# Kernel tuning notes

Hardware: AMD Instinct MI355X
Metric: run time of the kernel (lower is better)

## Reference

```python
import jax, jax.numpy as jnp
import numpy as np
import math

NUM_BUCKETS = 32
MAX_DISTANCE = 128


def _relative_position_bucket(relative_position):
    # Unidirectional (bidirectional=False): rp = max(-relative_position, 0)
    rp = jnp.maximum(-relative_position, 0)
    max_exact = NUM_BUCKETS // 2  # 16
    is_small = rp < max_exact
    rp_f = jnp.maximum(rp, 1).astype(jnp.float32)
    large = max_exact + (
        jnp.log(rp_f / max_exact) / math.log(MAX_DISTANCE / max_exact)
        * (NUM_BUCKETS - max_exact)
    ).astype(jnp.int32)
    large = jnp.minimum(large, NUM_BUCKETS - 1)
    return jnp.where(is_small, rp, large)


def _t5_rel_bias(bias_table, T):
    # bias_table: [num_buckets, n_heads] -> [1, n_heads, T, T]
    ctx = jnp.arange(T, dtype=jnp.int32)[:, None]
    mem = jnp.arange(T, dtype=jnp.int32)[None, :]
    buckets = _relative_position_bucket(mem - ctx)  # [T, T]
    values = bias_table[buckets]  # [T, T, H]
    return jnp.transpose(values, (2, 0, 1))[None]  # [1, H, T, T]


def setup_inputs() -> dict:
    key = jax.random.key(0)
    ks = jax.random.split(key, 6)
    B, T, C, H = 2, 2048, 1024, 16
    x = jax.random.normal(ks[0], (B, T, C), dtype=jnp.float32)
    W_attn = jax.random.normal(ks[1], (C, 3 * C), dtype=jnp.float32) * 0.02
    b_attn = jnp.zeros((3 * C,), dtype=jnp.float32)
    W_proj = jax.random.normal(ks[2], (C, C), dtype=jnp.float32) * 0.02
    b_proj = jnp.zeros((C,), dtype=jnp.float32)
    bias_table = jax.random.normal(ks[3], (NUM_BUCKETS, H), dtype=jnp.float32) * 0.02
    return {"x": x, "W_attn": W_attn, "b_attn": b_attn,
            "W_proj": W_proj, "b_proj": b_proj, "bias_table": bias_table}


def reference(x, W_attn, b_attn, W_proj, b_proj, bias_table):
    B, T, C = x.shape
    H = bias_table.shape[1]
    D = C // H
    qkv = x @ W_attn + b_attn  # [B, T, 3C]
    q, k, v = jnp.split(qkv, 3, axis=-1)
    # [B, T, C] -> [B, H, T, D]
    q = q.reshape(B, T, H, D).transpose(0, 2, 1, 3)
    k = k.reshape(B, T, H, D).transpose(0, 2, 1, 3)
    v = v.reshape(B, T, H, D).transpose(0, 2, 1, 3)
    rel_bias = _t5_rel_bias(bias_table, T)  # [1, H, T, T]
    att = jnp.einsum('bhtd,bhsd->bhts', q, k) * (1.0 / math.sqrt(D))
    att = att + rel_bias
    causal = jnp.tril(jnp.ones((T, T), dtype=bool))
    att = jnp.where(causal, att, -jnp.inf)
    att = jax.nn.softmax(att, axis=-1)
    y = jnp.einsum('bhts,bhsd->bhtd', att, v)  # [B, H, T, D]
    y = y.transpose(0, 2, 1, 3).reshape(B, T, C)
    return y @ W_proj + b_proj
```

## Files before the change

kernel.cpp:

```cpp
#include <hip/hip_runtime.h>
#include <hip/hip_bf16.h>
#include <math.h>

typedef __attribute__((ext_vector_type(4))) float f32x4;
typedef __attribute__((ext_vector_type(16))) float f32x16;
typedef __attribute__((ext_vector_type(8))) __bf16 bf16x8;
typedef __attribute__((ext_vector_type(4))) __bf16 bf16x4;
typedef __attribute__((ext_vector_type(4))) unsigned int u32x4;
typedef __attribute__((ext_vector_type(2))) unsigned int u32x2;

#define DEVI __device__ __forceinline__

DEVI f32x4 mfma16(bf16x8 a, bf16x8 b, f32x4 c) {
  return __builtin_amdgcn_mfma_f32_16x16x32_bf16(a, b, c, 0, 0, 0);
}
DEVI f32x16 mfma32(bf16x8 a, bf16x8 b, f32x16 c) {
  return __builtin_amdgcn_mfma_f32_32x32x16_bf16(a, b, c, 0, 0, 0);
}

DEVI void gload16(const void* g, void* l) {
  __builtin_amdgcn_global_load_lds(
      (const __attribute__((address_space(1))) void*)g,
      (__attribute__((address_space(3))) void*)l, 16, 0, 0);
}

DEVI float exp2a(float x) {
  float r;
  asm("v_exp_f32 %0, %1" : "=v"(r) : "v"(x));
  return r;
}
DEVI unsigned cvtpk(float lo, float hi) {
  unsigned r;
  asm("v_cvt_pk_bf16_f32 %0, %1, %2" : "=v"(r) : "v"(lo), "v"(hi));
  return r;
}

#define LOG2E 1.4426950408889634f
#define QSCALE 0.18033688011110793f
#define FIXMAX 8.0f

__global__ __launch_bounds__(256) void prep_k(
    const float* __restrict__ x, const float* __restrict__ W_attn,
    const float* __restrict__ W_proj, const float* __restrict__ bt,
    __bf16* __restrict__ xb, __bf16* __restrict__ WaT,
    __bf16* __restrict__ WpT, float* __restrict__ tbl) {
  __shared__ float tile[32][33];
  int bid = blockIdx.x;
  const int t = threadIdx.x;
  if (bid < 4096) {
    int i = (bid * 256 + t) * 4;
    float4 v = *(const float4*)&x[i];
    bf16x4 o = {(__bf16)v.x, (__bf16)v.y, (__bf16)v.z, (__bf16)v.w};
    *(bf16x4*)&xb[i] = o;
    return;
  }
  bid -= 4096;
  if (bid < 4096) {
    const float* in;
    __bf16* out;
    int Cc, bx, by;
    if (bid < 3072) {
      in = W_attn; out = WaT; Cc = 3072; bx = bid % 96; by = bid / 96;
    } else {
      int b2 = bid - 3072;
      in = W_proj; out = WpT; Cc = 1024; bx = b2 % 32; by = b2 / 32;
    }
    const int R = 1024;
    int tx = t & 31, ty = t >> 5;
    int xcol = bx * 32 + tx;
    for (int r = ty; r < 32; r += 8)
      tile[r][tx] = in[(size_t)(by * 32 + r) * Cc + xcol];
    __syncthreads();
    int xo = by * 32 + tx;
    for (int r = ty; r < 32; r += 8)
      out[(size_t)(bx * 32 + r) * R + xo] = (__bf16)tile[tx][r];
    return;
  }
  bid -= 4096;
  int idx = bid * 256 + t;
  int h = idx >> 11, rp = idx & 2047;
  int bucket;
  if (rp < 16) {
    bucket = rp;
  } else {
    float v = (logf((float)rp * 0.0625f) / 2.0794415416798357f) * 16.0f;
    bucket = 16 + (int)v;
    if (bucket > 31) bucket = 31;
  }
  tbl[idx] = bt[bucket * 16 + h] * LOG2E;
}

__global__ __launch_bounds__(256) void gemm_qkv(
    const __bf16* __restrict__ A, const __bf16* __restrict__ BT,
    const float* __restrict__ bias,
    __bf16* __restrict__ qb, __bf16* __restrict__ kb, __bf16* __restrict__ vtb,
    int M, int N, int K) {
  __shared__ __align__(16) __bf16 lA[2][128 * 32];
  __shared__ __align__(16) __bf16 lB[2][128 * 32];
  const int t = threadIdx.x;
  const int w = t >> 6, lane = t & 63;
  const int m0 = blockIdx.x * 128, n0 = blockIdx.y * 128;
  const int wr = (w >> 1) * 64, wc = (w & 1) * 64;

  f32x4 acc[4][4] = {};

  const int rA = lane & 15;
  const int kk = (lane >> 4) * 8;

  auto STAGE = [&](int buf, int k0) {
#pragma unroll
    for (int r = 0; r < 2; ++r) {
      int c = r * 256 + t;
      int row = c >> 2, cc = c & 3;
      gload16(A + (size_t)(m0 + row) * K + k0 + cc * 8,
              &lA[buf][(r * 256 + w * 64) * 8]);
      gload16(BT + (size_t)(n0 + row) * K + k0 + cc * 8,
              &lB[buf][(r * 256 + w * 64) * 8]);
    }
  };

  STAGE(0, 0);
  int cur = 0;
  for (int k0 = 0; k0 < K; k0 += 32, cur ^= 1) {
    __syncthreads();
    if (k0 + 32 < K) STAGE(cur ^ 1, k0 + 32);
    bf16x8 af[4], bfr[4];
#pragma unroll
    for (int i = 0; i < 4; ++i)
      af[i] = *(const bf16x8*)&lA[cur][(wr + i * 16 + rA) * 32 + kk];
#pragma unroll
    for (int j = 0; j < 4; ++j)
      bfr[j] = *(const bf16x8*)&lB[cur][(wc + j * 16 + rA) * 32 + kk];
#pragma unroll
    for (int i = 0; i < 4; ++i)
#pragma unroll
      for (int j = 0; j < 4; ++j)
        acc[i][j] = mfma16(af[i], bfr[j], acc[i][j]);
  }

  const int colb = n0 + wc + rA;
  const int rowb = m0 + wr + (lane >> 4) * 4;
#pragma unroll
  for (int j = 0; j < 4; ++j) {
    int n = colb + j * 16;
    float bv = bias[n];
#pragma unroll
    for (int i = 0; i < 4; ++i) {
#pragma unroll
      for (int e = 0; e < 4; ++e) {
        int m = rowb + i * 16 + e;
        float v = acc[i][j][e] + bv;
        int b = m >> 11, tt = m & 2047;
        int sec = n >> 10, nn = n & 1023;
        int h = nn >> 6, d = nn & 63;
        if (sec == 0)
          qb[(((size_t)(b * 16 + h)) * 2048 + tt) * 64 + d] = (__bf16)(v * QSCALE);
        else if (sec == 1)
          kb[(((size_t)(b * 16 + h)) * 2048 + tt) * 64 + d] = (__bf16)v;
        else
          vtb[(((size_t)(b * 16 + h)) * 64 + d) * 2048 + tt] = (__bf16)v;
      }
    }
  }
}

__global__ __launch_bounds__(256) void gemm_proj(
    const __bf16* __restrict__ A, const __bf16* __restrict__ BT,
    const float* __restrict__ bias, float* __restrict__ outF,
    int M, int N, int K) {
  __shared__ __align__(16) __bf16 lA[2][64 * 32];
  __shared__ __align__(16) __bf16 lB[2][128 * 32];
  const int t = threadIdx.x;
  const int w = t >> 6, lane = t & 63;
  const int m0 = blockIdx.x * 64, n0 = blockIdx.y * 128;
  const int wr = (w >> 1) * 32, wc = (w & 1) * 64;

  f32x4 acc[2][4] = {};

  const int rA = lane & 15;
  const int kk = (lane >> 4) * 8;

  auto STAGE = [&](int buf, int k0) {
    {
      int row = t >> 2, cc = t & 3;
      gload16(A + (size_t)(m0 + row) * K + k0 + cc * 8,
              &lA[buf][(w * 64) * 8]);
    }
#pragma unroll
    for (int r = 0; r < 2; ++r) {
      int c = r * 256 + t;
      int row = c >> 2, cc = c & 3;
      gload16(BT + (size_t)(n0 + row) * K + k0 + cc * 8,
              &lB[buf][(r * 256 + w * 64) * 8]);
    }
  };

  STAGE(0, 0);
  int cur = 0;
  for (int k0 = 0; k0 < K; k0 += 32, cur ^= 1) {
    __syncthreads();
    if (k0 + 32 < K) STAGE(cur ^ 1, k0 + 32);
    bf16x8 af[2], bfr[4];
#pragma unroll
    for (int i = 0; i < 2; ++i)
      af[i] = *(const bf16x8*)&lA[cur][(wr + i * 16 + rA) * 32 + kk];
#pragma unroll
    for (int j = 0; j < 4; ++j)
      bfr[j] = *(const bf16x8*)&lB[cur][(wc + j * 16 + rA) * 32 + kk];
#pragma unroll
    for (int i = 0; i < 2; ++i)
#pragma unroll
      for (int j = 0; j < 4; ++j)
        acc[i][j] = mfma16(af[i], bfr[j], acc[i][j]);
  }

  const int colb = n0 + wc + rA;
  const int rowb = m0 + wr + (lane >> 4) * 4;
#pragma unroll
  for (int j = 0; j < 4; ++j) {
    int n = colb + j * 16;
    float bv = bias[n];
#pragma unroll
    for (int i = 0; i < 2; ++i) {
#pragma unroll
      for (int e = 0; e < 4; ++e) {
        int m = rowb + i * 16 + e;
        outF[(size_t)m * N + n] = acc[i][j][e] + bv;
      }
    }
  }
}

__global__ __launch_bounds__(256) void attn_k(
    const __bf16* __restrict__ q, const __bf16* __restrict__ k,
    const __bf16* __restrict__ vt, const float* __restrict__ tbl,
    __bf16* __restrict__ y) {
  __shared__ __align__(16) char smem[2 * 8192 + 2 * 8192 + 2 * 768];
  float* lbuf = (float*)(smem + 32768);

  const int t = threadIdx.x, w = t >> 6, lane = t & 63;
  const int bh = blockIdx.x, b = bh >> 4, h = bh & 15;
  const int qt64 = 31 - blockIdx.y;
  const int qs = w >> 1, ks = w & 1;
  const int ncol = lane & 31, hi = lane >> 5;
  const int swl = ncol & 7;

  const __bf16* qp = q + (size_t)bh * 2048 * 64;
  const __bf16* kp = k + (size_t)bh * 2048 * 64;
  const __bf16* vp = vt + (size_t)bh * 64 * 2048;
  const float* tb = tbl + h * 2048;
  const float bconst = tb[2047] - FIXMAX;

  bf16x8 qf[4];
  {
    const __bf16* qr = qp + (size_t)(qt64 * 64 + qs * 32 + ncol) * 64 + hi * 8;
#pragma unroll
    for (int dc = 0; dc < 4; ++dc) qf[dc] = *(const bf16x8*)(qr + dc * 16);
  }

  f32x16 O0 = {}, O1 = {};
  float lsum = 0.f;
  const int ibase = 95 + 32 * (qs - ks) - 4 * hi + ncol;

  auto STAGE = [&](int buf, int jt) {
#pragma unroll
    for (int r = 0; r < 2; ++r) {
      int c = r * 256 + t;
      int row = c >> 3, cc = c & 7;
      int sc = cc ^ (row & 7);
      gload16(kp + (size_t)(jt * 64 + row) * 64 + sc * 8,
              smem + buf * 8192 + (r * 256 + w * 64) * 16);
      gload16(vp + (size_t)row * 2048 + jt * 64 + sc * 8,
              smem + 16384 + buf * 8192 + (r * 256 + w * 64) * 16);
    }
    int dtj = qt64 - jt;
    if (dtj < 3 && t < 192) {
      int rb = dtj * 64 - 95 + t;
      lbuf[buf * 192 + t] = tb[rb < 0 ? 0 : rb] - FIXMAX;
    }
  };

  STAGE(0, 0);
  int cur = 0;
  for (int jt = 0; jt <= qt64; ++jt, cur ^= 1) {
    const int dt = qt64 - jt;
    const int rel = 2 * dt + qs - ks;
    __syncthreads();
    if (jt < qt64) STAGE(cur ^ 1, jt + 1);
    if (rel < 0) continue;

    const char* Kc = smem + cur * 8192;
    const char* Vc = smem + 16384 + cur * 8192;
    const float* lbc = lbuf + cur * 192;

    f32x16 s;
    if (rel >= 5) {
#pragma unroll
      for (int r = 0; r < 16; ++r) s[r] = bconst;
    } else {
#pragma unroll
      for (int r = 0; r < 16; ++r) {
        int cr8 = (r & 3) + 8 * (r >> 2);
        float v = lbc[ibase - cr8];
        if (rel == 0 && ncol < cr8 + 4 * hi) v = -1e30f;
        s[r] = v;
      }
    }
    const char* Kb = Kc + (ks * 32 + ncol) * 128;
#pragma unroll
    for (int dc = 0; dc < 4; ++dc) {
      bf16x8 kf = *(const bf16x8*)(Kb + (((dc * 2 + hi) ^ swl) << 4));
      s = mfma32(kf, qf[dc], s);
    }
    float p[16];
#pragma unroll
    for (int r = 0; r < 16; ++r) {
      p[r] = exp2a(s[r]);
      lsum += p[r];
    }
#pragma unroll
    for (int s16 = 0; s16 < 2; ++s16) {
      unsigned we0 = cvtpk(p[8 * s16 + 0], p[8 * s16 + 1]);
      unsigned we1 = cvtpk(p[8 * s16 + 2], p[8 * s16 + 3]);
      unsigned wo0 = cvtpk(p[8 * s16 + 4], p[8 * s16 + 5]);
      unsigned wo1 = cvtpk(p[8 * s16 + 6], p[8 * s16 + 7]);
      u32x2 r0 = __builtin_amdgcn_permlane32_swap(we0, wo0, false, false);
      u32x2 r1 = __builtin_amdgcn_permlane32_swap(we1, wo1, false, false);
      u32x4 aw = {r0[0], r1[0], r0[1], r1[1]};
      bf16x8 af = __builtin_bit_cast(bf16x8, aw);
#pragma unroll
      for (int db = 0; db < 2; ++db) {
        const char* Vb = Vc + (db * 32 + ncol) * 128;
        bf16x8 vf = *(const bf16x8*)(Vb +
            ((((ks * 2 + s16) * 2 + hi) ^ swl) << 4));
        if (db == 0) O0 = mfma32(af, vf, O0);
        else         O1 = mfma32(af, vf, O1);
      }
    }
  }

  lsum += __shfl_xor(lsum, 32);
  __syncthreads();
  float* ls = (float*)(smem + 32768);
  if (ks) {
    char* dst = smem + qs * 8192 + lane * 128;
#pragma unroll
    for (int c = 0; c < 4; ++c) {
      f32x4 v0 = {O0[4 * c], O0[4 * c + 1], O0[4 * c + 2], O0[4 * c + 3]};
      *(f32x4*)(dst + ((c ^ swl) << 4)) = v0;
      f32x4 v1 = {O1[4 * c], O1[4 * c + 1], O1[4 * c + 2], O1[4 * c + 3]};
      *(f32x4*)(dst + (((c + 4) ^ swl) << 4)) = v1;
    }
    ls[qs * 64 + lane] = lsum;
  }
  __syncthreads();
  if (!ks) {
    lsum += ls[qs * 64 + lane];
    const char* src = smem + qs * 8192 + lane * 128;
#pragma unroll
    for (int c = 0; c < 4; ++c) {
      f32x4 v0 = *(const f32x4*)(src + ((c ^ swl) << 4));
      f32x4 v1 = *(const f32x4*)(src + (((c + 4) ^ swl) << 4));
#pragma unroll
      for (int e = 0; e < 4; ++e) {
        O0[4 * c + e] += v0[e];
        O1[4 * c + e] += v1[e];
      }
    }
    float rinv = 1.0f / lsum;
#pragma unroll
    for (int r = 0; r < 16; ++r) {
      int cr = (r & 3) + 8 * (r >> 2) + 4 * hi;
      float ri = __shfl(rinv, cr);
      int row = qt64 * 64 + qs * 32 + cr;
      size_t base = ((size_t)(b * 2048 + row)) * 1024 + h * 64 + ncol;
      y[base]      = (__bf16)(O0[r] * ri);
      y[base + 32] = (__bf16)(O1[r] * ri);
    }
  }
}


extern "C" void kernel_launch(void* const* d_in, const int* in_sizes, int n_in,
                              void* d_out, int out_size, void* d_ws, size_t ws_size,
                              hipStream_t stream) {
  const float* x = (const float*)d_in[0];
  const float* W_attn = (const float*)d_in[1];
  const float* b_attn = (const float*)d_in[2];
  const float* W_proj = (const float*)d_in[3];
  const float* b_proj = (const float*)d_in[4];
  const float* bias_table = (const float*)d_in[5];
  float* out = (float*)d_out;

  char* ws = (char*)d_ws;
  __bf16* xb   = (__bf16*)(ws + 0);
  __bf16* WaT  = (__bf16*)(ws + 8388608);
  __bf16* WpT  = (__bf16*)(ws + 14680064);
  __bf16* qb   = (__bf16*)(ws + 16777216);
  __bf16* kb   = (__bf16*)(ws + 25165824);
  __bf16* vtb  = (__bf16*)(ws + 33554432);
  __bf16* yb   = (__bf16*)(ws + 41943040);
  float*  tbl  = (float*)(ws + 50331648);

  prep_k<<<8320, 256, 0, stream>>>(x, W_attn, W_proj, bias_table,
                                   xb, WaT, WpT, tbl);
  gemm_qkv<<<dim3(32, 24), 256, 0, stream>>>(xb, WaT, b_attn,
                                             qb, kb, vtb, 4096, 3072, 1024);
  attn_k<<<dim3(32, 32), 256, 0, stream>>>(qb, kb, vtb, tbl, yb);
  gemm_proj<<<dim3(64, 8), 256, 0, stream>>>(yb, WpT, b_proj, out,
                                             4096, 1024, 1024);
}
```

Baseline: 109.8 us.

## Rewrite QKV GEMM with 256x256 tiles, swizzled LDS and interleaved MFMA phases

Replaces the 128x128 QKV GEMM tile with a 256x256 block of 8 waves, a K step of 64 and 64KB per operand of double-buffered LDS using an XOR swizzle. The main loop is split into four barrier-separated phases that reload A/B fragments between MFMA bursts, raising wave priority during MFMA. The goal is more operand reuse per LDS byte and fewer bank conflicts. The cost is only 192 blocks for 256 CUs, so parallelism drops, and the tile size and problem shape are now hardcoded.

```diff
diff --git a/kernel.cpp b/kernel.cpp
--- a/kernel.cpp
+++ b/kernel.cpp
@@ -90,69 +90,143 @@
   tbl[idx] = bt[bucket * 16 + h] * LOG2E;
 }
 
-__global__ __launch_bounds__(256) void gemm_qkv(
+__global__ __launch_bounds__(512, 2) void gemm_qkv(
     const __bf16* __restrict__ A, const __bf16* __restrict__ BT,
     const float* __restrict__ bias,
-    __bf16* __restrict__ qb, __bf16* __restrict__ kb, __bf16* __restrict__ vtb,
-    int M, int N, int K) {
-  __shared__ __align__(16) __bf16 lA[2][128 * 32];
-  __shared__ __align__(16) __bf16 lB[2][128 * 32];
-  const int t = threadIdx.x;
-  const int w = t >> 6, lane = t & 63;
-  const int m0 = blockIdx.x * 128, n0 = blockIdx.y * 128;
-  const int wr = (w >> 1) * 64, wc = (w & 1) * 64;
-
-  f32x4 acc[4][4] = {};
-
+    __bf16* __restrict__ qb, __bf16* __restrict__ kb, __bf16* __restrict__ vtb) {
+  __shared__ __align__(16) char lAm[65536];
+  __shared__ __align__(16) char lBm[65536];
+  const int t = threadIdx.x, w = t >> 6, lane = t & 63;
+  const int wm = w >> 2, wn = w & 3;
+  const int m0 = blockIdx.x * 256, n0 = blockIdx.y * 256;
   const int rA = lane & 15;
-  const int kk = (lane >> 4) * 8;
-
-  auto STAGE = [&](int buf, int k0) {
-#pragma unroll
-    for (int r = 0; r < 2; ++r) {
-      int c = r * 256 + t;
-      int row = c >> 2, cc = c & 3;
-      gload16(A + (size_t)(m0 + row) * K + k0 + cc * 8,
-              &lA[buf][(r * 256 + w * 64) * 8]);
-      gload16(BT + (size_t)(n0 + row) * K + k0 + cc * 8,
-              &lB[buf][(r * 256 + w * 64) * 8]);
-    }
+  const int aoff = rA * 128 + (((lane >> 4) * 16) ^ ((rA & 4) ? 32 : 0));
+  const int bro = (wn & 1) * 8192;
+
+  int srw[2], scl[2];
+#pragma unroll
+  for (int r = 0; r < 2; ++r) {
+    int d = r * 8192 + w * 1024 + lane * 16;
+    int lg = d ^ ((lane & 32) ? 32 : 0);
+    srw[r] = lg >> 7;
+    scl[r] = (lg & 127) >> 1;
+  }
+
+  f32x4 acc[8][4] = {};
+
+  auto STG = [&](int buf, const __bf16* src, int rows0, int kk0, char* opm,
+                 int half) {
+#pragma unroll
+    for (int r = 0; r < 2; ++r)
+      gload16(src + (size_t)(rows0 + half * 128 + srw[r]) * 1024 + kk0 + scl[r],
+              opm + buf * 32768 + half * 16384 + r * 8192 + w * 1024);
   };
-
-  STAGE(0, 0);
-  int cur = 0;
-  for (int k0 = 0; k0 < K; k0 += 32, cur ^= 1) {
-    __syncthreads();
-    if (k0 + 32 < K) STAGE(cur ^ 1, k0 + 32);
-    bf16x8 af[4], bfr[4];
+  auto STGALL = [&](int buf, int kk0) {
+    STG(buf, A, m0, kk0, lAm, 0);
+    STG(buf, A, m0, kk0, lAm, 1);
+    STG(buf, BT, n0, kk0, lBm, 0);
+    STG(buf, BT, n0, kk0, lBm, 1);
+  };
+
+  STGALL(0, 0);
+  asm volatile("s_waitcnt vmcnt(0)" ::: "memory");
+  __builtin_amdgcn_s_barrier();
+
+  for (int kt = 0; kt < 16; ++kt) {
+    const int c = kt & 1;
+    const char* Ah = lAm + c * 32768 + wm * 16384;
+    const char* Bh = lBm + c * 32768 + (wn >> 1) * 16384 + bro;
+    bf16x8 af[4][2], bfr[2][2];
+
+#pragma unroll
+    for (int i = 0; i < 4; ++i) {
+      af[i][0] = *(const bf16x8*)(Ah + i * 2048 + aoff);
+      af[i][1] = *(const bf16x8*)(Ah + i * 2048 + 64 + aoff);
+    }
+#pragma unroll
+    for (int j = 0; j < 2; ++j) {
+      bfr[j][0] = *(const bf16x8*)(Bh + j * 2048 + aoff);
+      bfr[j][1] = *(const bf16x8*)(Bh + j * 2048 + 64 + aoff);
+    }
+    if (kt + 1 < 16) STGALL(c ^ 1, (kt + 1) * 64);
+    __builtin_amdgcn_s_barrier();
+    __builtin_amdgcn_s_setprio(1);
 #pragma unroll
     for (int i = 0; i < 4; ++i)
-      af[i] = *(const bf16x8*)&lA[cur][(wr + i * 16 + rA) * 32 + kk];
-#pragma unroll
-    for (int j = 0; j < 4; ++j)
-      bfr[j] = *(const bf16x8*)&lB[cur][(wc + j * 16 + rA) * 32 + kk];
+#pragma unroll
+      for (int j = 0; j < 2; ++j)
+#pragma unroll
+        for (int kc = 0; kc < 2; ++kc)
+          acc[i][j] = mfma16(af[i][kc], bfr[j][kc], acc[i][j]);
+    __builtin_amdgcn_s_setprio(0);
+    __builtin_amdgcn_s_barrier();
+
+#pragma unroll
+    for (int j = 0; j < 2; ++j) {
+      bfr[j][0] = *(const bf16x8*)(Bh + (2 + j) * 2048 + aoff);
+      bfr[j][1] = *(const bf16x8*)(Bh + (2 + j) * 2048 + 64 + aoff);
+    }
+    __builtin_amdgcn_s_barrier();
+    __builtin_amdgcn_s_setprio(1);
 #pragma unroll
     for (int i = 0; i < 4; ++i)
 #pragma unroll
-      for (int j = 0; j < 4; ++j)
-        acc[i][j] = mfma16(af[i], bfr[j], acc[i][j]);
-  }
-
-  const int colb = n0 + wc + rA;
-  const int rowb = m0 + wr + (lane >> 4) * 4;
+      for (int j = 0; j < 2; ++j)
+#pragma unroll
+        for (int kc = 0; kc < 2; ++kc)
+          acc[i][2 + j] = mfma16(af[i][kc], bfr[j][kc], acc[i][2 + j]);
+    __builtin_amdgcn_s_setprio(0);
+    __builtin_amdgcn_s_barrier();
+
+#pragma unroll
+    for (int i = 0; i < 4; ++i) {
+      af[i][0] = *(const bf16x8*)(Ah + (4 + i) * 2048 + aoff);
+      af[i][1] = *(const bf16x8*)(Ah + (4 + i) * 2048 + 64 + aoff);
+    }
+    __builtin_amdgcn_s_barrier();
+    __builtin_amdgcn_s_setprio(1);
+#pragma unroll
+    for (int i = 0; i < 4; ++i)
+#pragma unroll
+      for (int j = 0; j < 2; ++j)
+#pragma unroll
+        for (int kc = 0; kc < 2; ++kc)
+          acc[4 + i][2 + j] = mfma16(af[i][kc], bfr[j][kc], acc[4 + i][2 + j]);
+    __builtin_amdgcn_s_setprio(0);
+    __builtin_amdgcn_s_barrier();
+
+#pragma unroll
+    for (int j = 0; j < 2; ++j) {
+      bfr[j][0] = *(const bf16x8*)(Bh + j * 2048 + aoff);
+      bfr[j][1] = *(const bf16x8*)(Bh + j * 2048 + 64 + aoff);
+    }
+    __builtin_amdgcn_s_barrier();
+    __builtin_amdgcn_s_setprio(1);
+#pragma unroll
+    for (int i = 0; i < 4; ++i)
+#pragma unroll
+      for (int j = 0; j < 2; ++j)
+#pragma unroll
+        for (int kc = 0; kc < 2; ++kc)
+          acc[4 + i][j] = mfma16(af[i][kc], bfr[j][kc], acc[4 + i][j]);
+    __builtin_amdgcn_s_setprio(0);
+    if (kt + 1 < 16) asm volatile("s_waitcnt vmcnt(0)" ::: "memory");
+    __builtin_amdgcn_s_barrier();
+  }
+
 #pragma unroll
   for (int j = 0; j < 4; ++j) {
-    int n = colb + j * 16;
+    int n = n0 + wn * 64 + j * 16 + rA;
     float bv = bias[n];
-#pragma unroll
-    for (int i = 0; i < 4; ++i) {
+    int sec = n >> 10, nn = n & 1023;
+    int h = nn >> 6, d = nn & 63;
+#pragma unroll
+    for (int i = 0; i < 8; ++i) {
 #pragma unroll
       for (int e = 0; e < 4; ++e) {
-        int m = rowb + i * 16 + e;
+        int m = m0 + wm * 128 + i * 16 + (lane >> 4) * 4 + e;
         float v = acc[i][j][e] + bv;
         int b = m >> 11, tt = m & 2047;
-        int sec = n >> 10, nn = n & 1023;
-        int h = nn >> 6, d = nn & 63;
         if (sec == 0)
           qb[(((size_t)(b * 16 + h)) * 2048 + tt) * 64 + d] = (__bf16)(v * QSCALE);
         else if (sec == 1)
@@ -404,8 +478,7 @@
 
   prep_k<<<8320, 256, 0, stream>>>(x, W_attn, W_proj, bias_table,
                                    xb, WaT, WpT, tbl);
-  gemm_qkv<<<dim3(32, 24), 256, 0, stream>>>(xb, WaT, b_attn,
-                                             qb, kb, vtb, 4096, 3072, 1024);
+  gemm_qkv<<<dim3(16, 12), 512, 0, stream>>>(xb, WaT, b_attn, qb, kb, vtb);
   attn_k<<<dim3(32, 32), 256, 0, stream>>>(qb, kb, vtb, tbl, yb);
   gemm_proj<<<dim3(64, 8), 256, 0, stream>>>(yb, WpT, b_proj, out,
                                              4096, 1024, 1024);
```

Result: slower. 133.3 us (+21.4%).

## Halve attention block to two waves, each covering both query sub-tiles

Applied to the files above, without the earlier changes.

The attention kernel now launches 128 threads instead of 256. Each wave keeps Q fragments for both 32-row query halves and reuses one set of K/V fragments loaded from LDS for both. This cuts LDS reads of K and V per MFMA and reduces the number of waves per block. In exchange it doubles the accumulator and Q registers per wave, which may lower occupancy, and each thread now issues twice as many global-to-LDS staging loads.

```diff
diff --git a/kernel.cpp b/kernel.cpp
--- a/kernel.cpp
+++ b/kernel.cpp
@@ -231,7 +231,7 @@
   }
 }
 
-__global__ __launch_bounds__(256) void attn_k(
+__global__ __launch_bounds__(128) void attn_k(
     const __bf16* __restrict__ q, const __bf16* __restrict__ k,
     const __bf16* __restrict__ vt, const float* __restrict__ tbl,
     __bf16* __restrict__ y) {
@@ -241,7 +241,7 @@
   const int t = threadIdx.x, w = t >> 6, lane = t & 63;
   const int bh = blockIdx.x, b = bh >> 4, h = bh & 15;
   const int qt64 = 31 - blockIdx.y;
-  const int qs = w >> 1, ks = w & 1;
+  const int ks = w;
   const int ncol = lane & 31, hi = lane >> 5;
   const int swl = ncol & 7;
 
@@ -251,32 +251,38 @@
   const float* tb = tbl + h * 2048;
   const float bconst = tb[2047] - FIXMAX;
 
-  bf16x8 qf[4];
-  {
+  bf16x8 qf[2][4];
+#pragma unroll
+  for (int qs = 0; qs < 2; ++qs) {
     const __bf16* qr = qp + (size_t)(qt64 * 64 + qs * 32 + ncol) * 64 + hi * 8;
 #pragma unroll
-    for (int dc = 0; dc < 4; ++dc) qf[dc] = *(const bf16x8*)(qr + dc * 16);
-  }
-
-  f32x16 O0 = {}, O1 = {};
-  float lsum = 0.f;
-  const int ibase = 95 + 32 * (qs - ks) - 4 * hi + ncol;
+    for (int dc = 0; dc < 4; ++dc) qf[qs][dc] = *(const bf16x8*)(qr + dc * 16);
+  }
+
+  f32x16 O[2][2] = {};
+  float lsum[2] = {0.f, 0.f};
 
   auto STAGE = [&](int buf, int jt) {
 #pragma unroll
-    for (int r = 0; r < 2; ++r) {
-      int c = r * 256 + t;
+    for (int r = 0; r < 4; ++r) {
+      int c = r * 128 + t;
       int row = c >> 3, cc = c & 7;
       int sc = cc ^ (row & 7);
       gload16(kp + (size_t)(jt * 64 + row) * 64 + sc * 8,
-              smem + buf * 8192 + (r * 256 + w * 64) * 16);
+              smem + buf * 8192 + (r * 128 + w * 64) * 16);
       gload16(vp + (size_t)row * 2048 + jt * 64 + sc * 8,
-              smem + 16384 + buf * 8192 + (r * 256 + w * 64) * 16);
+              smem + 16384 + buf * 8192 + (r * 128 + w * 64) * 16);
     }
     int dtj = qt64 - jt;
-    if (dtj < 3 && t < 192) {
-      int rb = dtj * 64 - 95 + t;
-      lbuf[buf * 192 + t] = tb[rb < 0 ? 0 : rb] - FIXMAX;
+    if (dtj < 3) {
+#pragma unroll
+      for (int i = 0; i < 2; ++i) {
+        int idx = i * 128 + t;
+        if (idx < 192) {
+          int rb = dtj * 64 - 95 + idx;
+          lbuf[buf * 192 + idx] = tb[rb < 0 ? 0 : rb] - FIXMAX;
+        }
+      }
     }
   };
 
@@ -284,98 +290,114 @@
   int cur = 0;
   for (int jt = 0; jt <= qt64; ++jt, cur ^= 1) {
     const int dt = qt64 - jt;
-    const int rel = 2 * dt + qs - ks;
     __syncthreads();
     if (jt < qt64) STAGE(cur ^ 1, jt + 1);
-    if (rel < 0) continue;
 
     const char* Kc = smem + cur * 8192;
     const char* Vc = smem + 16384 + cur * 8192;
     const float* lbc = lbuf + cur * 192;
 
-    f32x16 s;
-    if (rel >= 5) {
-#pragma unroll
-      for (int r = 0; r < 16; ++r) s[r] = bconst;
-    } else {
+    bf16x8 kf[4], vf[4];
+    const char* Kb = Kc + (ks * 32 + ncol) * 128;
+#pragma unroll
+    for (int dc = 0; dc < 4; ++dc)
+      kf[dc] = *(const bf16x8*)(Kb + (((dc * 2 + hi) ^ swl) << 4));
+#pragma unroll
+    for (int s16 = 0; s16 < 2; ++s16)
+#pragma unroll
+      for (int db = 0; db < 2; ++db)
+        vf[s16 * 2 + db] = *(const bf16x8*)(Vc + (db * 32 + ncol) * 128 +
+            ((((ks * 2 + s16) * 2 + hi) ^ swl) << 4));
+
+#pragma unroll
+    for (int qs = 0; qs < 2; ++qs) {
+      const int rel = 2 * dt + qs - ks;
+      if (rel < 0) continue;
+
+      const int ibase = 95 + 32 * (qs - ks) - 4 * hi + ncol;
+      f32x16 s;
+      if (rel >= 5) {
+#pragma unroll
+        for (int r = 0; r < 16; ++r) s[r] = bconst;
+      } else {
+#pragma unroll
+        for (int r = 0; r < 16; ++r) {
+          int cr8 = (r & 3) + 8 * (r >> 2);
+          float v = lbc[ibase - cr8];
+          if (rel == 0 && ncol < cr8 + 4 * hi) v = -1e30f;
+          s[r] = v;
+        }
+      }
+#pragma unroll
+      for (int dc = 0; dc < 4; ++dc) s = mfma32(kf[dc], qf[qs][dc], s);
+      float p[16];
 #pragma unroll
       for (int r = 0; r < 16; ++r) {
-        int cr8 = (r & 3) + 8 * (r >> 2);
-        float v = lbc[ibase - cr8];
-        if (rel == 0 && ncol < cr8 + 4 * hi) v = -1e30f;
-        s[r] = v;
-      }
-    }
-    const char* Kb = Kc + (ks * 32 + ncol) * 128;
-#pragma unroll
-    for (int dc = 0; dc < 4; ++dc) {
-      bf16x8 kf = *(const bf16x8*)(Kb + (((dc * 2 + hi) ^ swl) << 4));
-      s = mfma32(kf, qf[dc], s);
-    }
-    float p[16];
-#pragma unroll
-    for (int r = 0; r < 16; ++r) {
-      p[r] = exp2a(s[r]);
-      lsum += p[r];
-    }
-#pragma unroll
-    for (int s16 = 0; s16 < 2; ++s16) {
-      unsigned we0 = cvtpk(p[8 * s16 + 0], p[8 * s16 + 1]);
-      unsigned we1 = cvtpk(p[8 * s16 + 2], p[8 * s16 + 3]);
-      unsigned wo0 = cvtpk(p[8 * s16 + 4], p[8 * s16 + 5]);
-      unsigned wo1 = cvtpk(p[8 * s16 + 6], p[8 * s16 + 7]);
-      u32x2 r0 = __builtin_amdgcn_permlane32_swap(we0, wo0, false, false);
-      u32x2 r1 = __builtin_amdgcn_permlane32_swap(we1, wo1, false, false);
-      u32x4 aw = {r0[0], r1[0], r0[1], r1[1]};
-      bf16x8 af = __builtin_bit_cast(bf16x8, aw);
-#pragma unroll
-      for (int db = 0; db < 2; ++db) {
-        const char* Vb = Vc + (db * 32 + ncol) * 128;
-        bf16x8 vf = *(const bf16x8*)(Vb +
-            ((((ks * 2 + s16) * 2 + hi) ^ swl) << 4));
-        if (db == 0) O0 = mfma32(af, vf, O0);
-        else         O1 = mfma32(af, vf, O1);
-      }
-    }
-  }
-
-  lsum += __shfl_xor(lsum, 32);
+        p[r] = exp2a(s[r]);
+        lsum[qs] += p[r];
+      }
+#pragma unroll
+      for (int s16 = 0; s16 < 2; ++s16) {
+        unsigned we0 = cvtpk(p[8 * s16 + 0], p[8 * s16 + 1]);
+        unsigned we1 = cvtpk(p[8 * s16 + 2], p[8 * s16 + 3]);
+        unsigned wo0 = cvtpk(p[8 * s16 + 4], p[8 * s16 + 5]);
+        unsigned wo1 = cvtpk(p[8 * s16 + 6], p[8 * s16 + 7]);
+        u32x2 r0 = __builtin_amdgcn_permlane32_swap(we0, wo0, false, false);
+        u32x2 r1 = __builtin_amdgcn_permlane32_swap(we1, wo1, false, false);
+        u32x4 aw = {r0[0], r1[0], r0[1], r1[1]};
+        bf16x8 af = __builtin_bit_cast(bf16x8, aw);
+        O[qs][0] = mfma32(af, vf[s16 * 2 + 0], O[qs][0]);
+        O[qs][1] = mfma32(af, vf[s16 * 2 + 1], O[qs][1]);
+      }
+    }
+  }
+
+#pragma unroll
+  for (int qs = 0; qs < 2; ++qs) lsum[qs] += __shfl_xor(lsum[qs], 32);
   __syncthreads();
   float* ls = (float*)(smem + 32768);
   if (ks) {
-    char* dst = smem + qs * 8192 + lane * 128;
-#pragma unroll
-    for (int c = 0; c < 4; ++c) {
-      f32x4 v0 = {O0[4 * c], O0[4 * c + 1], O0[4 * c + 2], O0[4 * c + 3]};
-      *(f32x4*)(dst + ((c ^ swl) << 4)) = v0;
-      f32x4 v1 = {O1[4 * c], O1[4 * c + 1], O1[4 * c + 2], O1[4 * c + 3]};
-      *(f32x4*)(dst + (((c + 4) ^ swl) << 4)) = v1;
-    }
-    ls[qs * 64 + lane] = lsum;
+#pragma unroll
+    for (int qs = 0; qs < 2; ++qs) {
+      char* dst = smem + qs * 8192 + lane * 128;
+#pragma unroll
+      for (int c = 0; c < 4; ++c) {
+        f32x4 v0 = {O[qs][0][4 * c], O[qs][0][4 * c + 1],
+                    O[qs][0][4 * c + 2], O[qs][0][4 * c + 3]};
+        *(f32x4*)(dst + ((c ^ swl) << 4)) = v0;
+        f32x4 v1 = {O[qs][1][4 * c], O[qs][1][4 * c + 1],
+                    O[qs][1][4 * c + 2], O[qs][1][4 * c + 3]};
+        *(f32x4*)(dst + (((c + 4) ^ swl) << 4)) = v1;
+      }
+      ls[qs * 64 + lane] = lsum[qs];
+    }
   }
   __syncthreads();
   if (!ks) {
-    lsum += ls[qs * 64 + lane];
-    const char* src = smem + qs * 8192 + lane * 128;
-#pragma unroll
-    for (int c = 0; c < 4; ++c) {
-      f32x4 v0 = *(const f32x4*)(src + ((c ^ swl) << 4));
-      f32x4 v1 = *(const f32x4*)(src + (((c + 4) ^ swl) << 4));
-#pragma unroll
-      for (int e = 0; e < 4; ++e) {
-        O0[4 * c + e] += v0[e];
-        O1[4 * c + e] += v1[e];
-      }
-    }
-    float rinv = 1.0f / lsum;
-#pragma unroll
-    for (int r = 0; r < 16; ++r) {
-      int cr = (r & 3) + 8 * (r >> 2) + 4 * hi;
-      float ri = __shfl(rinv, cr);
-      int row = qt64 * 64 + qs * 32 + cr;
-      size_t base = ((size_t)(b * 2048 + row)) * 1024 + h * 64 + ncol;
-      y[base]      = (__bf16)(O0[r] * ri);
-      y[base + 32] = (__bf16)(O1[r] * ri);
+#pragma unroll
+    for (int qs = 0; qs < 2; ++qs) {
+      float lt = lsum[qs] + ls[qs * 64 + lane];
+      const char* src = smem + qs * 8192 + lane * 128;
+#pragma unroll
+      for (int c = 0; c < 4; ++c) {
+        f32x4 v0 = *(const f32x4*)(src + ((c ^ swl) << 4));
+        f32x4 v1 = *(const f32x4*)(src + (((c + 4) ^ swl) << 4));
+#pragma unroll
+        for (int e = 0; e < 4; ++e) {
+          O[qs][0][4 * c + e] += v0[e];
+          O[qs][1][4 * c + e] += v1[e];
+        }
+      }
+      float rinv = 1.0f / lt;
+#pragma unroll
+      for (int r = 0; r < 16; ++r) {
+        int cr = (r & 3) + 8 * (r >> 2) + 4 * hi;
+        float ri = __shfl(rinv, cr);
+        int row = qt64 * 64 + qs * 32 + cr;
+        size_t base = ((size_t)(b * 2048 + row)) * 1024 + h * 64 + ncol;
+        y[base]      = (__bf16)(O[qs][0][r] * ri);
+        y[base + 32] = (__bf16)(O[qs][1][r] * ri);
+      }
     }
   }
 }
@@ -406,7 +428,7 @@
                                    xb, WaT, WpT, tbl);
   gemm_qkv<<<dim3(32, 24), 256, 0, stream>>>(xb, WaT, b_attn,
                                              qb, kb, vtb, 4096, 3072, 1024);
-  attn_k<<<dim3(32, 32), 256, 0, stream>>>(qb, kb, vtb, tbl, yb);
+  attn_k<<<dim3(32, 32), 128, 0, stream>>>(qb, kb, vtb, tbl, yb);
   gemm_proj<<<dim3(64, 8), 256, 0, stream>>>(yb, WpT, b_proj, out,
                                              4096, 1024, 1024);
 }
```

New measurement: 120.7 us. 1.1x slower.

## Split KV range of long causal query tiles across two blocks with combine kernel

Applied to the files above, without the earlier changes.

Long query tiles (upper half) are processed by two blocks, each covering half of the key range, writing unnormalized bf16 partial outputs and row sums to workspace; short tiles run as before. A new combine kernel sums the partials and normalizes, relying on the fixed softmax max so no rescaling is needed. This balances per-block work in the causal attention and raises block count, at the cost of an extra launch, extra global traffic and bf16 rounding of partials.

```diff
diff --git a/kernel.cpp b/kernel.cpp
--- a/kernel.cpp
+++ b/kernel.cpp
@@ -234,13 +234,24 @@
 __global__ __launch_bounds__(256) void attn_k(
     const __bf16* __restrict__ q, const __bf16* __restrict__ k,
     const __bf16* __restrict__ vt, const float* __restrict__ tbl,
-    __bf16* __restrict__ y) {
+    __bf16* __restrict__ y, __bf16* __restrict__ Opart,
+    float* __restrict__ Lpart) {
   __shared__ __align__(16) char smem[2 * 8192 + 2 * 8192 + 2 * 768];
   float* lbuf = (float*)(smem + 32768);
 
   const int t = threadIdx.x, w = t >> 6, lane = t & 63;
   const int bh = blockIdx.x, b = bh >> 4, h = bh & 15;
-  const int qt64 = 31 - blockIdx.y;
+  const int p = blockIdx.y;
+  int qt64, jt0, jtend;
+  if (p < 32) {
+    qt64 = 16 + (p >> 1);
+    int lenA = (qt64 + 2) >> 1;
+    if ((p & 1) == 0) { jt0 = 0; jtend = lenA - 1; }
+    else             { jt0 = lenA; jtend = qt64; }
+  } else {
+    qt64 = 47 - p;
+    jt0 = 0; jtend = qt64;
+  }
   const int qs = w >> 1, ks = w & 1;
   const int ncol = lane & 31, hi = lane >> 5;
   const int swl = ncol & 7;
@@ -280,13 +291,13 @@
     }
   };
 
-  STAGE(0, 0);
+  STAGE(0, jt0);
   int cur = 0;
-  for (int jt = 0; jt <= qt64; ++jt, cur ^= 1) {
+  for (int jt = jt0; jt <= jtend; ++jt, cur ^= 1) {
     const int dt = qt64 - jt;
     const int rel = 2 * dt + qs - ks;
     __syncthreads();
-    if (jt < qt64) STAGE(cur ^ 1, jt + 1);
+    if (jt < jtend) STAGE(cur ^ 1, jt + 1);
     if (rel < 0) continue;
 
     const char* Kc = smem + cur * 8192;
@@ -312,18 +323,18 @@
       bf16x8 kf = *(const bf16x8*)(Kb + (((dc * 2 + hi) ^ swl) << 4));
       s = mfma32(kf, qf[dc], s);
     }
-    float p[16];
+    float p2[16];
 #pragma unroll
     for (int r = 0; r < 16; ++r) {
-      p[r] = exp2a(s[r]);
-      lsum += p[r];
+      p2[r] = exp2a(s[r]);
+      lsum += p2[r];
     }
 #pragma unroll
     for (int s16 = 0; s16 < 2; ++s16) {
-      unsigned we0 = cvtpk(p[8 * s16 + 0], p[8 * s16 + 1]);
-      unsigned we1 = cvtpk(p[8 * s16 + 2], p[8 * s16 + 3]);
-      unsigned wo0 = cvtpk(p[8 * s16 + 4], p[8 * s16 + 5]);
-      unsigned wo1 = cvtpk(p[8 * s16 + 6], p[8 * s16 + 7]);
+      unsigned we0 = cvtpk(p2[8 * s16 + 0], p2[8 * s16 + 1]);
+      unsigned we1 = cvtpk(p2[8 * s16 + 2], p2[8 * s16 + 3]);
+      unsigned wo0 = cvtpk(p2[8 * s16 + 4], p2[8 * s16 + 5]);
+      unsigned wo1 = cvtpk(p2[8 * s16 + 6], p2[8 * s16 + 7]);
       u32x2 r0 = __builtin_amdgcn_permlane32_swap(we0, wo0, false, false);
       u32x2 r1 = __builtin_amdgcn_permlane32_swap(we1, wo1, false, false);
       u32x4 aw = {r0[0], r1[0], r0[1], r1[1]};
@@ -367,16 +378,49 @@
         O1[4 * c + e] += v1[e];
       }
     }
-    float rinv = 1.0f / lsum;
-#pragma unroll
-    for (int r = 0; r < 16; ++r) {
-      int cr = (r & 3) + 8 * (r >> 2) + 4 * hi;
-      float ri = __shfl(rinv, cr);
-      int row = qt64 * 64 + qs * 32 + cr;
-      size_t base = ((size_t)(b * 2048 + row)) * 1024 + h * 64 + ncol;
-      y[base]      = (__bf16)(O0[r] * ri);
-      y[base + 32] = (__bf16)(O1[r] * ri);
-    }
+    if (p < 32) {
+      __bf16* Op = Opart + ((size_t)(bh * 32 + p)) * 4096;
+      if (hi == 0) Lpart[(bh * 32 + p) * 64 + qs * 32 + ncol] = lsum;
+#pragma unroll
+      for (int r = 0; r < 16; ++r) {
+        int cr = (r & 3) + 8 * (r >> 2) + 4 * hi;
+        int rl = qs * 32 + cr;
+        Op[rl * 64 + ncol]      = (__bf16)O0[r];
+        Op[rl * 64 + 32 + ncol] = (__bf16)O1[r];
+      }
+    } else {
+      float rinv = 1.0f / lsum;
+#pragma unroll
+      for (int r = 0; r < 16; ++r) {
+        int cr = (r & 3) + 8 * (r >> 2) + 4 * hi;
+        float ri = __shfl(rinv, cr);
+        int row = qt64 * 64 + qs * 32 + cr;
+        size_t base = ((size_t)(b * 2048 + row)) * 1024 + h * 64 + ncol;
+        y[base]      = (__bf16)(O0[r] * ri);
+        y[base + 32] = (__bf16)(O1[r] * ri);
+      }
+    }
+  }
+}
+
+__global__ __launch_bounds__(256) void attn_combine(
+    const __bf16* __restrict__ Opart, const float* __restrict__ Lpart,
+    __bf16* __restrict__ y) {
+  const int blk = blockIdx.x;
+  const int bh = blk >> 4, qti = blk & 15;
+  const int b = bh >> 4, h = bh & 15;
+  const int qt = 16 + qti;
+  const size_t ia = ((size_t)(bh * 32 + qti * 2)) * 4096;
+  const float* La = Lpart + (bh * 32 + qti * 2) * 64;
+  const int t = threadIdx.x;
+#pragma unroll
+  for (int e = 0; e < 16; ++e) {
+    int idx = e * 256 + t;
+    int row = idx >> 6, col = idx & 63;
+    float o = (float)Opart[ia + idx] + (float)Opart[ia + 4096 + idx];
+    float l = La[row] + La[64 + row];
+    y[((size_t)(b * 2048 + qt * 64 + row)) * 1024 + h * 64 + col] =
+        (__bf16)(o / l);
   }
 }
 
@@ -401,12 +445,15 @@
   __bf16* vtb  = (__bf16*)(ws + 33554432);
   __bf16* yb   = (__bf16*)(ws + 41943040);
   float*  tbl  = (float*)(ws + 50331648);
+  __bf16* Opart = (__bf16*)(ws + 0);
+  float*  Lpart = (float*)(ws + 8388608);
 
   prep_k<<<8320, 256, 0, stream>>>(x, W_attn, W_proj, bias_table,
                                    xb, WaT, WpT, tbl);
   gemm_qkv<<<dim3(32, 24), 256, 0, stream>>>(xb, WaT, b_attn,
                                              qb, kb, vtb, 4096, 3072, 1024);
-  attn_k<<<dim3(32, 32), 256, 0, stream>>>(qb, kb, vtb, tbl, yb);
+  attn_k<<<dim3(32, 48), 256, 0, stream>>>(qb, kb, vtb, tbl, yb, Opart, Lpart);
+  attn_combine<<<512, 256, 0, stream>>>(Opart, Lpart, yb);
   gemm_proj<<<dim3(64, 8), 256, 0, stream>>>(yb, WpT, b_proj, out,
                                              4096, 1024, 1024);
 }
```

After: 112.8 us. +2.8%, slower.
